# Kernel tuning notes

Measured on AMD Instinct MI355X. Metric: run time of the kernel, lower is better.

The kernel has to match this reference:

```python
import jax, jax.numpy as jnp
import numpy as np

B, N, DIN, DOUT = 16, 256, 64, 64
TEMP = 2.0          # temperatures[0]
POOL_K = 0.5        # pool_ratios[0]
BN_EPS = 1e-5


def setup_inputs() -> dict:
    key = jax.random.key(0)
    ks = jax.random.split(key, 8)
    g = lambda i, shape: (jax.random.normal(ks[i], shape, jnp.float32) * 0.08)
    return {
        "x": jax.random.normal(ks[0], (B, N, DIN), jnp.float32),
        # GraphAttentionLayer params
        "W_att": g(1, (DIN, DOUT)), "b_att": jnp.zeros((DOUT,), jnp.float32),
        "att_w": g(2, (DOUT,)),                      # att_weight [DOUT,1] squeezed
        "W_pwa": g(3, (DIN, DOUT)), "b_pwa": jnp.zeros((DOUT,), jnp.float32),
        "W_pna": g(4, (DIN, DOUT)), "b_pna": jnp.zeros((DOUT,), jnp.float32),
        "bn_scale": jnp.ones((DOUT,), jnp.float32),
        "bn_bias": jnp.zeros((DOUT,), jnp.float32),
        # GraphPool params
        "pool_w": g(5, (DOUT,)), "pool_b": jnp.zeros((), jnp.float32),
    }


def reference(x, W_att, b_att, att_w, W_pwa, b_pwa, W_pna, b_pna,
              bn_scale, bn_bias, pool_w, pool_b):
    # --- GraphAttentionLayer (eval mode: dropout = identity) ---
    # pairwise node multiplication: [B, i, j, DIN]
    pm = x[:, :, None, :] * x[:, None, :, :]
    att = jnp.tanh(jnp.einsum('bijd,de->bije', pm, W_att) + b_att)   # [B,N,N,DOUT]
    logits = jnp.einsum('bije,e->bij', att, att_w) / TEMP            # [B,N,N]
    # torch softmax over dim=-2 of [B,i,j,1] == axis j (the aggregated axis)
    A = jax.nn.softmax(logits, axis=2)                               # [B,N,N]
    agg = jnp.einsum('bij,bjd->bid', A, x)                           # [B,N,DIN]
    h = (agg @ W_pwa + b_pwa) + (x @ W_pna + b_pna)                  # [B,N,DOUT]
    # BatchNorm1d eval with running_mean=0, running_var=1
    h = h * (bn_scale / jnp.sqrt(1.0 + BN_EPS)) + bn_bias
    h = jax.nn.selu(h)
    # --- GraphPool (eval mode: dropout = identity) ---
    scores = jax.nn.sigmoid(h @ pool_w + pool_b)                     # [B,N]
    k = max(int(N * POOL_K), 1)
    _, idx = jax.lax.top_k(scores, k)                                # [B,k]
    hw = h * scores[:, :, None]
    out = jnp.take_along_axis(hw, idx[:, :, None], axis=1)           # [B,k,DOUT]
    return out
```

## Files before the change

### kernel.cpp

```cpp
#include <hip/hip_runtime.h>
#include <math.h>

#define BB 16
#define NN 256
#define DD 64
#define KTOP 128

typedef short s16x8 __attribute__((ext_vector_type(8)));
typedef float f32x4 __attribute__((ext_vector_type(4)));

__device__ __forceinline__ unsigned asu(float f){ union{float f;unsigned u;}c; c.f=f; return c.u; }
__device__ __forceinline__ float asf(unsigned u){ union{unsigned u;float f;}c; c.u=u; return c.f; }

__global__ __launch_bounds__(256, 2) void k_logits(
    const float* __restrict__ x, const float* __restrict__ W_att,
    const float* __restrict__ b_att, const float* __restrict__ att_w,
    float* __restrict__ logits)
{
    const int ig = blockIdx.x;
    const int b  = blockIdx.y;
    const int tid = threadIdx.x;
    const int w = tid >> 6, lane = tid & 63;
    const int quad = lane >> 4, c16 = lane & 15;
    const int jb = w * 64;
    const int ibase = ig * 4;

    __shared__ float sWt[64 * 68];
    __shared__ float sXi[4 * 64];
    __shared__ float sLog[4][64];

    #pragma unroll
    for (int r = 0; r < 16; ++r) {
        int lin = r * 256 + tid;
        int d = lin >> 6, e = lin & 63;
        sWt[e * 68 + d] = W_att[lin];
    }
    sXi[tid] = x[(b * NN + ibase + (tid >> 6)) * DD + (tid & 63)];

    float baw[4], aww[4];
    #pragma unroll
    for (int et = 0; et < 4; ++et) {
        baw[et] = b_att[et * 16 + c16];
        aww[et] = att_w[et * 16 + c16];
    }

    s16x8 Ah[4][2], Al[4][2];
    #pragma unroll
    for (int jt = 0; jt < 4; ++jt) {
        #pragma unroll
        for (int ks = 0; ks < 2; ++ks) {
            const float* xr = &x[(b * NN + jb + jt * 16 + c16) * DD + ks * 32 + quad * 8];
            float4 a0 = *(const float4*)xr;
            float4 a1 = *(const float4*)(xr + 4);
            float av[8] = {a0.x,a0.y,a0.z,a0.w,a1.x,a1.y,a1.z,a1.w};
            s16x8 h, l;
            #pragma unroll
            for (int t = 0; t < 8; ++t) {
                unsigned u = asu(av[t]);
                h[t] = (short)(u >> 16);
                float lf = av[t] - asf(u & 0xffff0000u);
                l[t] = (short)(asu(lf) >> 16);
            }
            Ah[jt][ks] = h; Al[jt][ks] = l;
        }
    }
    __syncthreads();

    for (int ii = 0; ii < 4; ++ii) {
        float xi[2][8];
        #pragma unroll
        for (int ks = 0; ks < 2; ++ks) {
            const float* xr = &sXi[ii * 64 + ks * 32 + quad * 8];
            float4 c0 = *(const float4*)xr;
            float4 c1 = *(const float4*)(xr + 4);
            xi[ks][0]=c0.x; xi[ks][1]=c0.y; xi[ks][2]=c0.z; xi[ks][3]=c0.w;
            xi[ks][4]=c1.x; xi[ks][5]=c1.y; xi[ks][6]=c1.z; xi[ks][7]=c1.w;
        }

        f32x4 acc[4][4];
        #pragma unroll
        for (int jt = 0; jt < 4; ++jt)
            #pragma unroll
            for (int et = 0; et < 4; ++et)
                acc[jt][et] = (f32x4){0.f, 0.f, 0.f, 0.f};

        #pragma unroll
        for (int ks = 0; ks < 2; ++ks) {
            #pragma unroll
            for (int et = 0; et < 4; ++et) {
                const float* wrow = &sWt[(et * 16 + c16) * 68 + ks * 32 + quad * 8];
                float4 w0 = *(const float4*)wrow;
                float4 w1 = *(const float4*)(wrow + 4);
                float wv[8] = {w0.x,w0.y,w0.z,w0.w,w1.x,w1.y,w1.z,w1.w};
                s16x8 bh, bl;
                #pragma unroll
                for (int t = 0; t < 8; ++t) {
                    float v = wv[t] * xi[ks][t];
                    unsigned u = asu(v);
                    bh[t] = (short)(u >> 16);
                    float lf = v - asf(u & 0xffff0000u);
                    bl[t] = (short)(asu(lf) >> 16);
                }
                #pragma unroll
                for (int jt = 0; jt < 4; ++jt) {
                    acc[jt][et] = __builtin_amdgcn_mfma_f32_16x16x32_bf16(Ah[jt][ks], bh, acc[jt][et], 0, 0, 0);
                    acc[jt][et] = __builtin_amdgcn_mfma_f32_16x16x32_bf16(Al[jt][ks], bh, acc[jt][et], 0, 0, 0);
                    acc[jt][et] = __builtin_amdgcn_mfma_f32_16x16x32_bf16(Ah[jt][ks], bl, acc[jt][et], 0, 0, 0);
                }
            }
        }

        float p[4][4];
        #pragma unroll
        for (int jt = 0; jt < 4; ++jt)
            #pragma unroll
            for (int r = 0; r < 4; ++r) p[jt][r] = 0.0f;

        #pragma unroll
        for (int et = 0; et < 4; ++et) {
            #pragma unroll
            for (int jt = 0; jt < 4; ++jt) {
                #pragma unroll
                for (int r = 0; r < 4; ++r) {
                    float v = acc[jt][et][r] + baw[et];
                    float m = __expf(v + v);
                    float th = fmaf(-2.0f, __builtin_amdgcn_rcpf(m + 1.0f), 1.0f);
                    p[jt][r] = fmaf(aww[et], th, p[jt][r]);
                }
            }
        }

        #pragma unroll
        for (int jt = 0; jt < 4; ++jt) {
            #pragma unroll
            for (int r = 0; r < 4; ++r) {
                float s = p[jt][r];
                s += __shfl_xor(s, 1);
                s += __shfl_xor(s, 2);
                s += __shfl_xor(s, 4);
                s += __shfl_xor(s, 8);
                if (c16 == 0) sLog[w][jt * 16 + quad * 4 + r] = s;
            }
        }
        __asm__ volatile("s_waitcnt lgkmcnt(0)" ::: "memory");
        float lv = sLog[w][lane];
        logits[(b * NN + ibase + ii) * NN + jb + lane] = lv * 0.5f;
    }
}

__global__ __launch_bounds__(256) void k_soft(
    const float* __restrict__ x, const float* __restrict__ logits,
    const float* __restrict__ Wpwa, const float* __restrict__ bpwa,
    const float* __restrict__ Wpna, const float* __restrict__ bpna,
    const float* __restrict__ bnsc, const float* __restrict__ bnbi,
    const float* __restrict__ poolw, const float* __restrict__ poolb,
    float* __restrict__ hbuf, float* __restrict__ scores)
{
    const int bx   = blockIdx.x;
    const int b    = bx >> 6;
    const int ig   = bx & 63;
    const int w    = threadIdx.x >> 6;
    const int lane = threadIdx.x & 63;
    const int i    = ig * 4 + w;

    __shared__ float sA[4][256];
    __shared__ float sAgg[4][64];
    __shared__ float sXi[4][64];

    const float* row = &logits[((b * NN) + i) * NN];
    float lg0 = row[lane], lg1 = row[lane + 64], lg2 = row[lane + 128], lg3 = row[lane + 192];
    float m = fmaxf(fmaxf(lg0, lg1), fmaxf(lg2, lg3));
    #pragma unroll
    for (int off = 32; off; off >>= 1) m = fmaxf(m, __shfl_xor(m, off));
    float e0 = __expf(lg0 - m), e1 = __expf(lg1 - m), e2 = __expf(lg2 - m), e3 = __expf(lg3 - m);
    float ssum = e0 + e1 + e2 + e3;
    #pragma unroll
    for (int off = 32; off; off >>= 1) ssum += __shfl_xor(ssum, off);
    float inv = 1.0f / ssum;
    sA[w][lane] = e0 * inv; sA[w][lane + 64] = e1 * inv;
    sA[w][lane + 128] = e2 * inv; sA[w][lane + 192] = e3 * inv;
    sXi[w][lane] = x[((b * NN) + i) * DD + lane];
    __syncthreads();

    float agg = 0.0f;
    const float4* A4 = (const float4*)&sA[w][0];
    const float* xb = &x[(b * NN) * DD];
    #pragma unroll 4
    for (int jq = 0; jq < 64; ++jq) {
        float4 a = A4[jq];
        int j = jq * 4;
        agg = fmaf(a.x, xb[(j + 0) * DD + lane], agg);
        agg = fmaf(a.y, xb[(j + 1) * DD + lane], agg);
        agg = fmaf(a.z, xb[(j + 2) * DD + lane], agg);
        agg = fmaf(a.w, xb[(j + 3) * DD + lane], agg);
    }
    sAgg[w][lane] = agg;
    __syncthreads();

    double hacc = (double)bpwa[lane] + (double)bpna[lane];
    #pragma unroll 4
    for (int d = 0; d < 64; ++d) {
        hacc += (double)sAgg[w][d] * (double)Wpwa[d * DD + lane]
              + (double)sXi[w][d]  * (double)Wpna[d * DD + lane];
    }
    const double bnmul = 0.99999500003749968750e0;
    double hb = hacc * ((double)bnsc[lane] * bnmul) + (double)bnbi[lane];
    float hf = (float)hb;
    const float LAM = 1.0507009873554805f, ALP = 1.6732632423543772f;
    float hs = hf > 0.0f ? LAM * hf : LAM * ALP * (__expf(hf) - 1.0f);
    hbuf[((b * NN) + i) * DD + lane] = hs;

    double z = (double)hs * (double)poolw[lane];
    #pragma unroll
    for (int off = 32; off; off >>= 1) z += __shfl_xor(z, off);
    if (lane == 0) {
        double zz = z + (double)poolb[0];
        scores[b * NN + i] = (float)(1.0 / (1.0 + exp(-zz)));
    }
}

__global__ __launch_bounds__(256) void k_topk(
    const float* __restrict__ scores, const float* __restrict__ hbuf,
    float* __restrict__ out)
{
    const int b = blockIdx.x;
    const int t = threadIdx.x;
    __shared__ float ss[256];
    __shared__ int   si[256];
    ss[t] = scores[b * NN + t];
    si[t] = t;
    __syncthreads();
    for (int k = 2; k <= 256; k <<= 1) {
        for (int j = k >> 1; j > 0; j >>= 1) {
            int p = t ^ j;
            if (p > t) {
                float a = ss[t], c = ss[p];
                int ia = si[t], ic = si[p];
                bool desc = ((t & k) == 0);
                bool aFirst = (a > c) || (a == c && ia < ic);
                bool dosw = desc ? (!aFirst) : aFirst;
                if (dosw) { ss[t] = c; ss[p] = a; si[t] = ic; si[p] = ia; }
            }
            __syncthreads();
        }
    }
    for (int m = t; m < KTOP * DD; m += 256) {
        int r = m >> 6, e = m & 63;
        out[(b * KTOP + r) * DD + e] = hbuf[((b * NN) + si[r]) * DD + e] * ss[r];
    }
}

extern "C" void kernel_launch(void* const* d_in, const int* in_sizes, int n_in,
                              void* d_out, int out_size, void* d_ws, size_t ws_size,
                              hipStream_t stream) {
    const float* x        = (const float*)d_in[0];
    const float* W_att    = (const float*)d_in[1];
    const float* b_att    = (const float*)d_in[2];
    const float* att_w    = (const float*)d_in[3];
    const float* W_pwa    = (const float*)d_in[4];
    const float* b_pwa    = (const float*)d_in[5];
    const float* W_pna    = (const float*)d_in[6];
    const float* b_pna    = (const float*)d_in[7];
    const float* bn_scale = (const float*)d_in[8];
    const float* bn_bias  = (const float*)d_in[9];
    const float* pool_w   = (const float*)d_in[10];
    const float* pool_b   = (const float*)d_in[11];

    float* logits = (float*)d_ws;
    float* hbuf   = logits + BB * NN * NN;
    float* scoresW = hbuf + BB * NN * DD;
    float* out    = (float*)d_out;

    k_logits<<<dim3(64, BB), 256, 0, stream>>>(x, W_att, b_att, att_w, logits);
    k_soft<<<dim3(BB * 64), 256, 0, stream>>>(x, logits, W_pwa, b_pwa, W_pna, b_pna,
                                              bn_scale, bn_bias, pool_w, pool_b,
                                              hbuf, scoresW);
    k_topk<<<dim3(BB), 256, 0, stream>>>(scoresW, hbuf, out);
}
```

Before: 152.9 us.

## Fuse logits and softmax/aggregation kernels, keep logits in LDS

Merges the logits kernel with the softmax, aggregation, projection and pooling-score kernel, so logits stay in shared memory and are never written to or read back from global memory. Each block now handles 2 rows instead of 4, doubling the grid to keep occupancy up. The tanh exponent becomes an exp2 with prescaled constants, and the bf16 hi/lo split uses the packed float2-to-bf162 conversion (round-to-nearest instead of truncation). The cost is that half the waves sit idle during the softmax and epilogue phase, and each block reloads W_att and the x j-fragments twice as often.

```diff
diff --git a/kernel.cpp b/kernel.cpp
--- a/kernel.cpp
+++ b/kernel.cpp
@@ -1,4 +1,5 @@
 #include <hip/hip_runtime.h>
+#include <hip/hip_bf16.h>
 #include <math.h>
 
 #define BB 16
@@ -9,13 +10,28 @@
 typedef short s16x8 __attribute__((ext_vector_type(8)));
 typedef float f32x4 __attribute__((ext_vector_type(4)));
 
-__device__ __forceinline__ unsigned asu(float f){ union{float f;unsigned u;}c; c.f=f; return c.u; }
+typedef union { s16x8 v; unsigned u[4]; } frag_u;
+typedef union { __hip_bfloat162 b2; unsigned u; } cvu;
+
 __device__ __forceinline__ float asf(unsigned u){ union{unsigned u;float f;}c; c.u=u; return c.f; }
 
-__global__ __launch_bounds__(256, 2) void k_logits(
+__device__ __forceinline__ void split2(float v0, float v1, unsigned& hu, unsigned& lu) {
+    cvu c; c.b2 = __float22bfloat162_rn(make_float2(v0, v1));
+    unsigned h = c.u;
+    float l0 = v0 - asf(h << 16);
+    float l1 = v1 - asf(h & 0xffff0000u);
+    c.b2 = __float22bfloat162_rn(make_float2(l0, l1));
+    hu = h; lu = c.u;
+}
+
+__global__ __launch_bounds__(256, 2) void k_fused(
     const float* __restrict__ x, const float* __restrict__ W_att,
     const float* __restrict__ b_att, const float* __restrict__ att_w,
-    float* __restrict__ logits)
+    const float* __restrict__ Wpwa, const float* __restrict__ bpwa,
+    const float* __restrict__ Wpna, const float* __restrict__ bpna,
+    const float* __restrict__ bnsc, const float* __restrict__ bnbi,
+    const float* __restrict__ poolw, const float* __restrict__ poolb,
+    float* __restrict__ hbuf, float* __restrict__ scores)
 {
     const int ig = blockIdx.x;
     const int b  = blockIdx.y;
@@ -23,11 +39,12 @@
     const int w = tid >> 6, lane = tid & 63;
     const int quad = lane >> 4, c16 = lane & 15;
     const int jb = w * 64;
-    const int ibase = ig * 4;
+    const int ibase = ig * 2;
 
     __shared__ float sWt[64 * 68];
-    __shared__ float sXi[4 * 64];
-    __shared__ float sLog[4][64];
+    __shared__ float sXi[2 * 64];
+    __shared__ float sL[2][256];
+    __shared__ float sAgg[2][64];
 
     #pragma unroll
     for (int r = 0; r < 16; ++r) {
@@ -35,16 +52,17 @@
         int d = lin >> 6, e = lin & 63;
         sWt[e * 68 + d] = W_att[lin];
     }
-    sXi[tid] = x[(b * NN + ibase + (tid >> 6)) * DD + (tid & 63)];
-
-    float baw[4], aww[4];
+    if (tid < 128) sXi[tid] = x[(b * NN + ibase + (tid >> 6)) * DD + (tid & 63)];
+
+    const float L2E2 = 2.8853900817779268f;
+    float bawL[4], aww[4];
     #pragma unroll
     for (int et = 0; et < 4; ++et) {
-        baw[et] = b_att[et * 16 + c16];
-        aww[et] = att_w[et * 16 + c16];
-    }
-
-    s16x8 Ah[4][2], Al[4][2];
+        bawL[et] = b_att[et * 16 + c16] * L2E2;
+        aww[et]  = att_w[et * 16 + c16];
+    }
+
+    frag_u Ah[4][2], Al[4][2];
     #pragma unroll
     for (int jt = 0; jt < 4; ++jt) {
         #pragma unroll
@@ -52,21 +70,15 @@
             const float* xr = &x[(b * NN + jb + jt * 16 + c16) * DD + ks * 32 + quad * 8];
             float4 a0 = *(const float4*)xr;
             float4 a1 = *(const float4*)(xr + 4);
-            float av[8] = {a0.x,a0.y,a0.z,a0.w,a1.x,a1.y,a1.z,a1.w};
-            s16x8 h, l;
-            #pragma unroll
-            for (int t = 0; t < 8; ++t) {
-                unsigned u = asu(av[t]);
-                h[t] = (short)(u >> 16);
-                float lf = av[t] - asf(u & 0xffff0000u);
-                l[t] = (short)(asu(lf) >> 16);
-            }
-            Ah[jt][ks] = h; Al[jt][ks] = l;
+            split2(a0.x, a0.y, Ah[jt][ks].u[0], Al[jt][ks].u[0]);
+            split2(a0.z, a0.w, Ah[jt][ks].u[1], Al[jt][ks].u[1]);
+            split2(a1.x, a1.y, Ah[jt][ks].u[2], Al[jt][ks].u[2]);
+            split2(a1.z, a1.w, Ah[jt][ks].u[3], Al[jt][ks].u[3]);
         }
     }
     __syncthreads();
 
-    for (int ii = 0; ii < 4; ++ii) {
+    for (int ii = 0; ii < 2; ++ii) {
         float xi[2][8];
         #pragma unroll
         for (int ks = 0; ks < 2; ++ks) {
@@ -91,21 +103,16 @@
                 const float* wrow = &sWt[(et * 16 + c16) * 68 + ks * 32 + quad * 8];
                 float4 w0 = *(const float4*)wrow;
                 float4 w1 = *(const float4*)(wrow + 4);
-                float wv[8] = {w0.x,w0.y,w0.z,w0.w,w1.x,w1.y,w1.z,w1.w};
-                s16x8 bh, bl;
-                #pragma unroll
-                for (int t = 0; t < 8; ++t) {
-                    float v = wv[t] * xi[ks][t];
-                    unsigned u = asu(v);
-                    bh[t] = (short)(u >> 16);
-                    float lf = v - asf(u & 0xffff0000u);
-                    bl[t] = (short)(asu(lf) >> 16);
-                }
+                frag_u bh, bl;
+                split2(w0.x * xi[ks][0], w0.y * xi[ks][1], bh.u[0], bl.u[0]);
+                split2(w0.z * xi[ks][2], w0.w * xi[ks][3], bh.u[1], bl.u[1]);
+                split2(w1.x * xi[ks][4], w1.y * xi[ks][5], bh.u[2], bl.u[2]);
+                split2(w1.z * xi[ks][6], w1.w * xi[ks][7], bh.u[3], bl.u[3]);
                 #pragma unroll
                 for (int jt = 0; jt < 4; ++jt) {
-                    acc[jt][et] = __builtin_amdgcn_mfma_f32_16x16x32_bf16(Ah[jt][ks], bh, acc[jt][et], 0, 0, 0);
-                    acc[jt][et] = __builtin_amdgcn_mfma_f32_16x16x32_bf16(Al[jt][ks], bh, acc[jt][et], 0, 0, 0);
-                    acc[jt][et] = __builtin_amdgcn_mfma_f32_16x16x32_bf16(Ah[jt][ks], bl, acc[jt][et], 0, 0, 0);
+                    acc[jt][et] = __builtin_amdgcn_mfma_f32_16x16x32_bf16(Ah[jt][ks].v, bh.v, acc[jt][et], 0, 0, 0);
+                    acc[jt][et] = __builtin_amdgcn_mfma_f32_16x16x32_bf16(Al[jt][ks].v, bh.v, acc[jt][et], 0, 0, 0);
+                    acc[jt][et] = __builtin_amdgcn_mfma_f32_16x16x32_bf16(Ah[jt][ks].v, bl.v, acc[jt][et], 0, 0, 0);
                 }
             }
         }
@@ -122,8 +129,8 @@
             for (int jt = 0; jt < 4; ++jt) {
                 #pragma unroll
                 for (int r = 0; r < 4; ++r) {
-                    float v = acc[jt][et][r] + baw[et];
-                    float m = __expf(v + v);
+                    float arg = fmaf(acc[jt][et][r], L2E2, bawL[et]);
+                    float m = __builtin_amdgcn_exp2f(arg);
                     float th = fmaf(-2.0f, __builtin_amdgcn_rcpf(m + 1.0f), 1.0f);
                     p[jt][r] = fmaf(aww[et], th, p[jt][r]);
                 }
@@ -139,83 +146,63 @@
                 s += __shfl_xor(s, 2);
                 s += __shfl_xor(s, 4);
                 s += __shfl_xor(s, 8);
-                if (c16 == 0) sLog[w][jt * 16 + quad * 4 + r] = s;
-            }
-        }
+                if (c16 == 0) sL[ii][jb + jt * 16 + quad * 4 + r] = s * 0.5f;
+            }
+        }
+    }
+    __syncthreads();
+
+    if (w < 2) {
+        const int i = ibase + w;
+        float* row = sL[w];
+        float lg0 = row[lane], lg1 = row[lane + 64], lg2 = row[lane + 128], lg3 = row[lane + 192];
+        float m = fmaxf(fmaxf(lg0, lg1), fmaxf(lg2, lg3));
+        #pragma unroll
+        for (int off = 32; off; off >>= 1) m = fmaxf(m, __shfl_xor(m, off));
+        float e0 = __expf(lg0 - m), e1 = __expf(lg1 - m), e2 = __expf(lg2 - m), e3 = __expf(lg3 - m);
+        float ssum = e0 + e1 + e2 + e3;
+        #pragma unroll
+        for (int off = 32; off; off >>= 1) ssum += __shfl_xor(ssum, off);
+        float inv = 1.0f / ssum;
+        row[lane] = e0 * inv; row[lane + 64] = e1 * inv;
+        row[lane + 128] = e2 * inv; row[lane + 192] = e3 * inv;
         __asm__ volatile("s_waitcnt lgkmcnt(0)" ::: "memory");
-        float lv = sLog[w][lane];
-        logits[(b * NN + ibase + ii) * NN + jb + lane] = lv * 0.5f;
-    }
-}
-
-__global__ __launch_bounds__(256) void k_soft(
-    const float* __restrict__ x, const float* __restrict__ logits,
-    const float* __restrict__ Wpwa, const float* __restrict__ bpwa,
-    const float* __restrict__ Wpna, const float* __restrict__ bpna,
-    const float* __restrict__ bnsc, const float* __restrict__ bnbi,
-    const float* __restrict__ poolw, const float* __restrict__ poolb,
-    float* __restrict__ hbuf, float* __restrict__ scores)
-{
-    const int bx   = blockIdx.x;
-    const int b    = bx >> 6;
-    const int ig   = bx & 63;
-    const int w    = threadIdx.x >> 6;
-    const int lane = threadIdx.x & 63;
-    const int i    = ig * 4 + w;
-
-    __shared__ float sA[4][256];
-    __shared__ float sAgg[4][64];
-    __shared__ float sXi[4][64];
-
-    const float* row = &logits[((b * NN) + i) * NN];
-    float lg0 = row[lane], lg1 = row[lane + 64], lg2 = row[lane + 128], lg3 = row[lane + 192];
-    float m = fmaxf(fmaxf(lg0, lg1), fmaxf(lg2, lg3));
-    #pragma unroll
-    for (int off = 32; off; off >>= 1) m = fmaxf(m, __shfl_xor(m, off));
-    float e0 = __expf(lg0 - m), e1 = __expf(lg1 - m), e2 = __expf(lg2 - m), e3 = __expf(lg3 - m);
-    float ssum = e0 + e1 + e2 + e3;
-    #pragma unroll
-    for (int off = 32; off; off >>= 1) ssum += __shfl_xor(ssum, off);
-    float inv = 1.0f / ssum;
-    sA[w][lane] = e0 * inv; sA[w][lane + 64] = e1 * inv;
-    sA[w][lane + 128] = e2 * inv; sA[w][lane + 192] = e3 * inv;
-    sXi[w][lane] = x[((b * NN) + i) * DD + lane];
-    __syncthreads();
-
-    float agg = 0.0f;
-    const float4* A4 = (const float4*)&sA[w][0];
-    const float* xb = &x[(b * NN) * DD];
-    #pragma unroll 4
-    for (int jq = 0; jq < 64; ++jq) {
-        float4 a = A4[jq];
-        int j = jq * 4;
-        agg = fmaf(a.x, xb[(j + 0) * DD + lane], agg);
-        agg = fmaf(a.y, xb[(j + 1) * DD + lane], agg);
-        agg = fmaf(a.z, xb[(j + 2) * DD + lane], agg);
-        agg = fmaf(a.w, xb[(j + 3) * DD + lane], agg);
-    }
-    sAgg[w][lane] = agg;
-    __syncthreads();
-
-    double hacc = (double)bpwa[lane] + (double)bpna[lane];
-    #pragma unroll 4
-    for (int d = 0; d < 64; ++d) {
-        hacc += (double)sAgg[w][d] * (double)Wpwa[d * DD + lane]
-              + (double)sXi[w][d]  * (double)Wpna[d * DD + lane];
-    }
-    const double bnmul = 0.99999500003749968750e0;
-    double hb = hacc * ((double)bnsc[lane] * bnmul) + (double)bnbi[lane];
-    float hf = (float)hb;
-    const float LAM = 1.0507009873554805f, ALP = 1.6732632423543772f;
-    float hs = hf > 0.0f ? LAM * hf : LAM * ALP * (__expf(hf) - 1.0f);
-    hbuf[((b * NN) + i) * DD + lane] = hs;
-
-    double z = (double)hs * (double)poolw[lane];
-    #pragma unroll
-    for (int off = 32; off; off >>= 1) z += __shfl_xor(z, off);
-    if (lane == 0) {
-        double zz = z + (double)poolb[0];
-        scores[b * NN + i] = (float)(1.0 / (1.0 + exp(-zz)));
+
+        float agg = 0.0f;
+        const float4* A4 = (const float4*)row;
+        const float* xb = &x[(b * NN) * DD];
+        #pragma unroll 8
+        for (int jq = 0; jq < 64; ++jq) {
+            float4 a = A4[jq];
+            int j = jq * 4;
+            agg = fmaf(a.x, xb[(j + 0) * DD + lane], agg);
+            agg = fmaf(a.y, xb[(j + 1) * DD + lane], agg);
+            agg = fmaf(a.z, xb[(j + 2) * DD + lane], agg);
+            agg = fmaf(a.w, xb[(j + 3) * DD + lane], agg);
+        }
+        sAgg[w][lane] = agg;
+        __asm__ volatile("s_waitcnt lgkmcnt(0)" ::: "memory");
+
+        double hacc = (double)bpwa[lane] + (double)bpna[lane];
+        #pragma unroll 4
+        for (int d = 0; d < 64; ++d) {
+            hacc += (double)sAgg[w][d] * (double)Wpwa[d * DD + lane]
+                  + (double)sXi[w * 64 + d] * (double)Wpna[d * DD + lane];
+        }
+        const double bnmul = 0.99999500003749968750e0;
+        double hb = hacc * ((double)bnsc[lane] * bnmul) + (double)bnbi[lane];
+        float hf = (float)hb;
+        const float LAM = 1.0507009873554805f, ALP = 1.6732632423543772f;
+        float hs = hf > 0.0f ? LAM * hf : LAM * ALP * (__expf(hf) - 1.0f);
+        hbuf[((b * NN) + i) * DD + lane] = hs;
+
+        double z = (double)hs * (double)poolw[lane];
+        #pragma unroll
+        for (int off = 32; off; off >>= 1) z += __shfl_xor(z, off);
+        if (lane == 0) {
+            double zz = z + (double)poolb[0];
+            scores[b * NN + i] = (float)(1.0 / (1.0 + exp(-zz)));
+        }
     }
 }
 
@@ -266,14 +253,13 @@
     const float* pool_w   = (const float*)d_in[10];
     const float* pool_b   = (const float*)d_in[11];
 
-    float* logits = (float*)d_ws;
-    float* hbuf   = logits + BB * NN * NN;
+    float* hbuf    = (float*)d_ws;
     float* scoresW = hbuf + BB * NN * DD;
-    float* out    = (float*)d_out;
-
-    k_logits<<<dim3(64, BB), 256, 0, stream>>>(x, W_att, b_att, att_w, logits);
-    k_soft<<<dim3(BB * 64), 256, 0, stream>>>(x, logits, W_pwa, b_pwa, W_pna, b_pna,
-                                              bn_scale, bn_bias, pool_w, pool_b,
-                                              hbuf, scoresW);
+    float* out     = (float*)d_out;
+
+    k_fused<<<dim3(128, BB), 256, 0, stream>>>(x, W_att, b_att, att_w,
+                                               W_pwa, b_pwa, W_pna, b_pna,
+                                               bn_scale, bn_bias, pool_w, pool_b,
+                                               hbuf, scoresW);
     k_topk<<<dim3(BB), 256, 0, stream>>>(scoresW, hbuf, out);
 }
```

Measured after the change: 177.0 us. +15.8%, slower.
